# Performance work log

Hardware: AMD Instinct MI355X
Metric: run time of the kernel (lower is better)

Reference implementation:

```python
import jax, jax.numpy as jnp
import numpy as np

N_NODES = 100000
N_EDGES = 400000
F_IN = 128
HEADS = 4
C1 = 64   # conv1 out per head
C2 = 128  # conv2 out per head
G = 2048  # num graphs
FP = 2048
HID = 64
NEG_SLOPE = 0.2


def _gat_conv(x, edge_index, W, a_src, a_dst, b, heads, ch):
    """PyG-style GATConv with self-loops, concat=True."""
    n = x.shape[0]
    loops = jnp.arange(n, dtype=edge_index.dtype)
    src = jnp.concatenate([edge_index[0], loops])
    dst = jnp.concatenate([edge_index[1], loops])
    h = (x @ W).reshape(n, heads, ch)                      # [N,H,C]
    e_src = jnp.sum(h * a_src, axis=-1)                    # [N,H]
    e_dst = jnp.sum(h * a_dst, axis=-1)                    # [N,H]
    logits = jax.nn.leaky_relu(e_src[src] + e_dst[dst], NEG_SLOPE)  # [E,H]
    m = jax.ops.segment_max(logits, dst, num_segments=n)   # per-dst max
    p = jnp.exp(logits - m[dst])
    denom = jax.ops.segment_sum(p, dst, num_segments=n)
    alpha = p / denom[dst]                                 # [E,H]
    out = jax.ops.segment_sum(h[src] * alpha[:, :, None], dst, num_segments=n)
    return out.reshape(n, heads * ch) + b


def setup_inputs() -> dict:
    key = jax.random.key(0)
    ks = jax.random.split(key, 16)
    s = 0.05
    inp = {
        "x": jax.random.normal(ks[0], (N_NODES, F_IN), jnp.float32),
        "edge_index": jax.random.randint(ks[1], (2, N_EDGES), 0, N_NODES, jnp.int32),
        "batch": jnp.sort(jax.random.randint(ks[2], (N_NODES,), 0, G, jnp.int32)),
        "fp": jax.random.normal(ks[3], (G, FP), jnp.float32),
        "W1": jax.random.normal(ks[4], (F_IN, HEADS * C1), jnp.float32) * s,
        "a_src1": jax.random.normal(ks[5], (HEADS, C1), jnp.float32) * s,
        "a_dst1": jax.random.normal(ks[6], (HEADS, C1), jnp.float32) * s,
        "b1": jnp.zeros((HEADS * C1,), jnp.float32),
        "W2": jax.random.normal(ks[7], (HEADS * C1, HEADS * C2), jnp.float32) * s,
        "a_src2": jax.random.normal(ks[8], (HEADS, C2), jnp.float32) * s,
        "a_dst2": jax.random.normal(ks[9], (HEADS, C2), jnp.float32) * s,
        "b2": jnp.zeros((HEADS * C2,), jnp.float32),
        "Wfp": jax.random.normal(ks[10], (FP, HID), jnp.float32) * s,
        "bfp": jnp.zeros((HID,), jnp.float32),
        "Wfc1": jax.random.normal(ks[11], (HEADS * C2 + HID, HID), jnp.float32) * s,
        "bfc1": jnp.zeros((HID,), jnp.float32),
        "Wfc2": jax.random.normal(ks[12], (HID, 1), jnp.float32) * s,
        "bfc2": jnp.zeros((1,), jnp.float32),
    }
    return inp


def reference(x, edge_index, batch, fp, W1, a_src1, a_dst1, b1, W2, a_src2, a_dst2, b2,
              Wfp, bfp, Wfc1, bfc1, Wfc2, bfc2):
    h = _gat_conv(x, edge_index, W1, a_src1, a_dst1, b1, HEADS, C1)
    h = jax.nn.elu(h)
    h = _gat_conv(h, edge_index, W2, a_src2, a_dst2, b2, HEADS, C2)
    h = jax.nn.elu(h)
    # global mean pool over graphs
    sums = jax.ops.segment_sum(h, batch, num_segments=G)
    counts = jax.ops.segment_sum(jnp.ones((h.shape[0], 1), h.dtype), batch, num_segments=G)
    pooled = sums / jnp.maximum(counts, 1.0)               # [G, 512]
    fph = fp @ Wfp + bfp                                   # [G, 64]
    z = jnp.concatenate([pooled, fph], axis=1)             # [G, 576]
    z = jax.nn.relu(z @ Wfc1 + bfc1)
    # dropout is identity in eval mode
    return z @ Wfc2 + bfc2                                 # [G, 1]
```

## Files before the change

### kernel.cpp

```cpp
#include <hip/hip_runtime.h>
#include <math.h>

#define NEG_SLOPE 0.2f

typedef __attribute__((ext_vector_type(8))) short bf16x8;
typedef __attribute__((ext_vector_type(4))) float f32x4;
typedef __attribute__((ext_vector_type(2))) float f32x2;

__device__ __forceinline__ float b2f(short s) {
  return __uint_as_float(((unsigned int)(unsigned short)s) << 16);
}
__device__ __forceinline__ unsigned short f2b_rne(float f) {
  unsigned int u = __float_as_uint(f);
  u = (u + 0x7FFF + ((u >> 16) & 1)) >> 16;
  return (unsigned short)u;
}

__device__ __forceinline__ void fp8x8_to_f32(uint2 raw, float* f) {
  f32x2 a = __builtin_amdgcn_cvt_pk_f32_fp8((int)raw.x, false);
  f32x2 b = __builtin_amdgcn_cvt_pk_f32_fp8((int)raw.x, true);
  f32x2 c = __builtin_amdgcn_cvt_pk_f32_fp8((int)raw.y, false);
  f32x2 d = __builtin_amdgcn_cvt_pk_f32_fp8((int)raw.y, true);
  f[0] = a[0]; f[1] = a[1]; f[2] = b[0]; f[3] = b[1];
  f[4] = c[0]; f[5] = c[1]; f[6] = d[0]; f[7] = d[1];
}

__device__ __forceinline__ void tr_one(const float* __restrict__ W,
                                       unsigned short* __restrict__ WT,
                                       int K, int N, int idx)
{
  if (idx < K * N) {
    int k = idx / N, n = idx - k * N;
    WT[(size_t)n * K + k] = f2b_rne(W[idx]);
  }
}

__global__ __launch_bounds__(256) void prep_all(
    const float* __restrict__ x, unsigned short* __restrict__ xb, size_t nx, int B0,
    const float* __restrict__ fp, unsigned short* __restrict__ fpb, size_t nf, int B1,
    const float* __restrict__ W1, unsigned short* __restrict__ W1T,
    const float* __restrict__ W2, unsigned short* __restrict__ W2T,
    const float* __restrict__ Wfp, unsigned short* __restrict__ WfpT,
    const float* __restrict__ Wfc1, unsigned short* __restrict__ Wfc1T)
{
  int b = blockIdx.x;
  const int t = threadIdx.x;
  if (b < B0) {
    size_t i = (size_t)b * 256 + t;
    if (i < nx) xb[i] = f2b_rne(x[i]);
    return;
  }
  b -= B0;
  if (b < B1) {
    size_t i = (size_t)b * 256 + t;
    if (i < nf) fpb[i] = f2b_rne(fp[i]);
    return;
  }
  b -= B1;
  if (b < 128) { tr_one(W1, W1T, 128, 256, b * 256 + t); return; }
  b -= 128;
  if (b < 512) { tr_one(W2, W2T, 256, 512, b * 256 + t); return; }
  b -= 512;
  if (b < 512) { tr_one(Wfp, WfpT, 2048, 64, b * 256 + t); return; }
  b -= 512;
  tr_one(Wfc1, Wfc1T, 576, 64, b * 256 + t);
}

template<int EMODE>
__global__ __launch_bounds__(256) void gemm_mfma(
    const unsigned short* __restrict__ A, const unsigned short* __restrict__ BT,
    unsigned char* __restrict__ Cout, int M, int N, int K,
    const float* __restrict__ a_src, const float* __restrict__ a_dst,
    float* __restrict__ es, float* __restrict__ ed, int nh)
{
  const int LDT = 40;
  __shared__ unsigned short As[128 * 40];
  __shared__ unsigned short Bs[128 * 40];
  const int tid  = threadIdx.x;
  const int wave = tid >> 6;
  const int lane = tid & 63;
  const int ln   = lane & 15;
  const int quad = lane >> 4;
  const int wr0  = (wave >> 1) * 64;
  const int wc0  = (wave & 1) * 64;
  const int bm   = blockIdx.y * 128;
  const int bn   = blockIdx.x * 128;
  const int srow  = tid >> 2;
  const int skoff = (tid & 3) * 8;

  f32x4 acc[4][4];
  const f32x4 z4 = {0.f, 0.f, 0.f, 0.f};
#pragma unroll
  for (int i = 0; i < 4; ++i)
#pragma unroll
    for (int j = 0; j < 4; ++j) acc[i][j] = z4;

  const bf16x8 zb8 = {0, 0, 0, 0, 0, 0, 0, 0};
  bf16x8 pa[2] = {zb8, zb8}, pb[2] = {zb8, zb8};
  bf16x8 na[2] = {zb8, zb8}, nb[2] = {zb8, zb8};
#pragma unroll
  for (int p = 0; p < 2; ++p) {
    int r = srow + p * 64;
    pa[p] = (bm + r < M) ? *(const bf16x8*)(A + (size_t)(bm + r) * K + skoff) : zb8;
    pb[p] = *(const bf16x8*)(BT + (size_t)(bn + r) * K + skoff);
  }

  for (int k0 = 0; k0 < K; k0 += 32) {
#pragma unroll
    for (int p = 0; p < 2; ++p) {
      int r = srow + p * 64;
      *(bf16x8*)(&As[r * LDT + skoff]) = pa[p];
      *(bf16x8*)(&Bs[r * LDT + skoff]) = pb[p];
    }
    __syncthreads();
    if (k0 + 32 < K) {
      int kn = k0 + 32;
#pragma unroll
      for (int p = 0; p < 2; ++p) {
        int r = srow + p * 64;
        na[p] = (bm + r < M) ? *(const bf16x8*)(A + (size_t)(bm + r) * K + kn + skoff) : zb8;
        nb[p] = *(const bf16x8*)(BT + (size_t)(bn + r) * K + kn + skoff);
      }
    }
    bf16x8 af[4], bfv[4];
#pragma unroll
    for (int i = 0; i < 4; ++i)
      af[i] = *(const bf16x8*)(&As[(wr0 + i * 16 + ln) * LDT + quad * 8]);
#pragma unroll
    for (int j = 0; j < 4; ++j)
      bfv[j] = *(const bf16x8*)(&Bs[(wc0 + j * 16 + ln) * LDT + quad * 8]);
#pragma unroll
    for (int i = 0; i < 4; ++i)
#pragma unroll
      for (int j = 0; j < 4; ++j)
        acc[i][j] = __builtin_amdgcn_mfma_f32_16x16x32_bf16(af[i], bfv[j], acc[i][j], 0, 0, 0);
    __syncthreads();
#pragma unroll
    for (int p = 0; p < 2; ++p) { pa[p] = na[p]; pb[p] = nb[p]; }
  }

#pragma unroll
  for (int i = 0; i < 4; ++i) {
#pragma unroll
    for (int r = 0; r < 4; ++r) {
      int row = bm + wr0 + i * 16 + quad * 4 + r;
      if (row >= M) continue;
      int p01 = __builtin_amdgcn_cvt_pk_fp8_f32(acc[i][0][r], acc[i][1][r], 0, false);
      int p23 = __builtin_amdgcn_cvt_pk_fp8_f32(acc[i][2][r], acc[i][3][r], 0, false);
      size_t rb = (size_t)row * N + bn + wc0 + ln;
      Cout[rb +  0] = (unsigned char)(p01 & 0xff);
      Cout[rb + 16] = (unsigned char)((p01 >> 8) & 0xff);
      Cout[rb + 32] = (unsigned char)(p23 & 0xff);
      Cout[rb + 48] = (unsigned char)((p23 >> 8) & 0xff);
    }
  }

  float asv[4], adv[4];
#pragma unroll
  for (int j = 0; j < 4; ++j) {
    int col = bn + wc0 + j * 16 + ln;
    asv[j] = a_src[col];
    adv[j] = a_dst[col];
  }
  if (EMODE == 64) {
    const int head = (bn + wc0) >> 6;
#pragma unroll
    for (int i = 0; i < 4; ++i) {
#pragma unroll
      for (int r = 0; r < 4; ++r) {
        float ps = 0.f, pd = 0.f;
#pragma unroll
        for (int j = 0; j < 4; ++j) {
          ps = fmaf(acc[i][j][r], asv[j], ps);
          pd = fmaf(acc[i][j][r], adv[j], pd);
        }
        for (int off = 8; off; off >>= 1) {
          ps += __shfl_down(ps, off, 16);
          pd += __shfl_down(pd, off, 16);
        }
        if (ln == 0) {
          int row = bm + wr0 + i * 16 + quad * 4 + r;
          if (row < M) {
            es[(size_t)row * nh + head] = ps;
            ed[(size_t)row * nh + head] = pd;
          }
        }
      }
    }
  } else {
    float* esp = (float*)As;
    float* edp = esp + 256;
#pragma unroll
    for (int i = 0; i < 4; ++i) {
#pragma unroll
      for (int r = 0; r < 4; ++r) {
        float ps = 0.f, pd = 0.f;
#pragma unroll
        for (int j = 0; j < 4; ++j) {
          ps = fmaf(acc[i][j][r], asv[j], ps);
          pd = fmaf(acc[i][j][r], adv[j], pd);
        }
        for (int off = 8; off; off >>= 1) {
          ps += __shfl_down(ps, off, 16);
          pd += __shfl_down(pd, off, 16);
        }
        if (ln == 0) {
          int rl = wr0 + i * 16 + quad * 4 + r;
          esp[rl * 2 + (wc0 >> 6)] = ps;
          edp[rl * 2 + (wc0 >> 6)] = pd;
        }
      }
    }
    __syncthreads();
    if (tid < 128) {
      int row = bm + tid;
      if (row < M) {
        int head = bn >> 7;
        es[(size_t)row * nh + head] = esp[tid * 2] + esp[tid * 2 + 1];
        ed[(size_t)row * nh + head] = edp[tid * 2] + edp[tid * 2 + 1];
      }
    }
  }
}

__global__ __launch_bounds__(256) void gemm_mfma_n64(
    const unsigned short* __restrict__ A, int lda,
    const unsigned short* __restrict__ BT, int ldb,
    float* __restrict__ Cp, int M, int kchunk)
{
  const int LDT = 72;
  __shared__ unsigned short As[128 * 72];
  __shared__ unsigned short Bs[64 * 72];
  const int tid  = threadIdx.x;
  const int wave = tid >> 6;
  const int lane = tid & 63;
  const int ln   = lane & 15;
  const int quad = lane >> 4;
  const int ks   = blockIdx.x;
  const int bm   = blockIdx.y * 128;
  const int k_beg = ks * kchunk;
  const int k_end = k_beg + kchunk;
  const int arow = tid >> 1;
  const int akb  = (tid & 1) * 32;
  const int brow = tid >> 2;
  const int bkb  = (tid & 3) * 16;

  f32x4 acc[2][4];
  const f32x4 z4 = {0.f, 0.f, 0.f, 0.f};
#pragma unroll
  for (int i = 0; i < 2; ++i)
#pragma unroll
    for (int j = 0; j < 4; ++j) acc[i][j] = z4;

  for (int k0 = k_beg; k0 < k_end; k0 += 64) {
    const unsigned short* ap = A + (size_t)(bm + arow) * lda + k0 + akb;
#pragma unroll
    for (int q = 0; q < 4; ++q)
      *(bf16x8*)(&As[arow * LDT + akb + q * 8]) = *(const bf16x8*)(ap + q * 8);
    const unsigned short* bp = BT + (size_t)brow * ldb + k0 + bkb;
#pragma unroll
    for (int q = 0; q < 2; ++q)
      *(bf16x8*)(&Bs[brow * LDT + bkb + q * 8]) = *(const bf16x8*)(bp + q * 8);
    __syncthreads();
#pragma unroll
    for (int kk = 0; kk < 2; ++kk) {
      bf16x8 af[2], bfv[4];
#pragma unroll
      for (int i = 0; i < 2; ++i)
        af[i] = *(const bf16x8*)(&As[(wave * 32 + i * 16 + ln) * LDT + kk * 32 + quad * 8]);
#pragma unroll
      for (int j = 0; j < 4; ++j)
        bfv[j] = *(const bf16x8*)(&Bs[(j * 16 + ln) * LDT + kk * 32 + quad * 8]);
#pragma unroll
      for (int i = 0; i < 2; ++i)
#pragma unroll
        for (int j = 0; j < 4; ++j)
          acc[i][j] = __builtin_amdgcn_mfma_f32_16x16x32_bf16(af[i], bfv[j], acc[i][j], 0, 0, 0);
    }
    __syncthreads();
  }
#pragma unroll
  for (int i = 0; i < 2; ++i)
#pragma unroll
    for (int r = 0; r < 4; ++r) {
      int row = bm + wave * 32 + i * 16 + quad * 4 + r;
#pragma unroll
      for (int j = 0; j < 4; ++j)
        Cp[((size_t)ks * M + row) * 64 + j * 16 + ln] = acc[i][j][r];
    }
}

__global__ void fp_finish(const float* __restrict__ Cp, int ksplit, int M,
                          const float* __restrict__ bfp,
                          unsigned short* __restrict__ zb)
{
  const int g = blockIdx.x;
  const int j = threadIdx.x;
  float s = bfp[j];
  for (int ks = 0; ks < ksplit; ++ks) s += Cp[((size_t)ks * M + g) * 64 + j];
  zb[(size_t)g * 576 + 512 + j] = f2b_rne(s);
}

__global__ void mlp_finish(const float* __restrict__ Cp, int ksplit, int M,
                           const float* __restrict__ bfc1,
                           const float* __restrict__ Wfc2, const float* __restrict__ bfc2,
                           float* __restrict__ out)
{
  const int g = blockIdx.x;
  const int j = threadIdx.x;
  float s = bfc1[j];
  for (int ks = 0; ks < ksplit; ++ks) s += Cp[((size_t)ks * M + g) * 64 + j];
  s = s > 0.f ? s : 0.f;
  float term = s * Wfc2[j];
  for (int off = 32; off; off >>= 1) term += __shfl_down(term, off, 64);
  if (j == 0) out[g] = term + bfc2[0];
}

__global__ void count_all(const int* __restrict__ ei, int E, int* __restrict__ deg,
                          const int* __restrict__ batch, int NN, int* __restrict__ gcnt,
                          int BE)
{
  int b = blockIdx.x;
  int t = threadIdx.x;
  if (b < BE) {
    int e = b * 256 + t;
    if (e < E) atomicAdd(&deg[ei[E + e]], 1);
  } else {
    int i = (b - BE) * 256 + t;
    if (i < NN) atomicAdd(&gcnt[batch[i]], 1);
  }
}

__global__ void fill_csr(const int* __restrict__ ei, int E, int* __restrict__ cursor,
                         const int* __restrict__ rowptr, int* __restrict__ csr_src)
{
  int e = blockIdx.x * 256 + threadIdx.x;
  if (e < E) {
    int d = ei[E + e];
    int pos = atomicAdd(&cursor[d], 1);
    csr_src[rowptr[d] + pos] = ei[e];
  }
}

__device__ void scan_p1_body(const int* __restrict__ vals, int n, int* __restrict__ bsum,
                             int bb)
{
  __shared__ int red[256];
  int base = bb * 1024;
  int t = threadIdx.x;
  int s = 0;
#pragma unroll
  for (int i = 0; i < 4; ++i) {
    int idx = base + i * 256 + t;
    if (idx < n) s += vals[idx];
  }
  red[t] = s;
  __syncthreads();
  for (int off = 128; off; off >>= 1) {
    if (t < off) red[t] += red[t + off];
    __syncthreads();
  }
  if (t == 0) bsum[bb] = red[0];
}

__global__ void scan2_p1(const int* __restrict__ vA, int nA, int* __restrict__ bsA, int nbA,
                         const int* __restrict__ vB, int nB, int* __restrict__ bsB)
{
  int b = blockIdx.x;
  if (b < nbA) scan_p1_body(vA, nA, bsA, b);
  else         scan_p1_body(vB, nB, bsB, b - nbA);
}

__device__ void scan_p2_body(const int* __restrict__ bsum, int* __restrict__ bpre,
                             int nb, int* __restrict__ rowptr, int n)
{
  __shared__ int tmp[128];
  int t = threadIdx.x;
  int v = (t < nb) ? bsum[t] : 0;
  tmp[t] = v;
  __syncthreads();
  for (int off = 1; off < 128; off <<= 1) {
    int add = (t >= off) ? tmp[t - off] : 0;
    __syncthreads();
    tmp[t] += add;
    __syncthreads();
  }
  if (t < nb) bpre[t] = tmp[t] - v;
  if (t == 127) rowptr[n] = tmp[127];
}

__global__ void scan2_p2(const int* __restrict__ bsA, int* __restrict__ bpA, int nbA,
                         int* __restrict__ rpA, int nA,
                         const int* __restrict__ bsB, int* __restrict__ bpB, int nbB,
                         int* __restrict__ rpB, int nB)
{
  if (blockIdx.x == 0) scan_p2_body(bsA, bpA, nbA, rpA, nA);
  else                 scan_p2_body(bsB, bpB, nbB, rpB, nB);
}

__device__ void scan_p3_body(const int* __restrict__ vals, const int* __restrict__ bpre,
                             int n, int* __restrict__ rowptr, int bb)
{
  __shared__ int tmp[256];
  int t = threadIdx.x;
  int base = bb * 1024 + t * 4;
  int v[4]; int s = 0;
#pragma unroll
  for (int i = 0; i < 4; ++i) {
    int idx = base + i;
    v[i] = (idx < n) ? vals[idx] : 0;
    s += v[i];
  }
  tmp[t] = s;
  __syncthreads();
  for (int off = 1; off < 256; off <<= 1) {
    int add = (t >= off) ? tmp[t - off] : 0;
    __syncthreads();
    tmp[t] += add;
    __syncthreads();
  }
  int run = bpre[bb] + tmp[t] - s;
#pragma unroll
  for (int i = 0; i < 4; ++i) {
    int idx = base + i;
    if (idx < n) rowptr[idx] = run;
    run += v[i];
  }
}

__global__ void scan2_p3(const int* __restrict__ vA, const int* __restrict__ bpA, int nA,
                         int* __restrict__ rpA, int nbA,
                         const int* __restrict__ vB, const int* __restrict__ bpB, int nB,
                         int* __restrict__ rpB)
{
  int b = blockIdx.x;
  if (b < nbA) scan_p3_body(vA, bpA, nA, rpA, b);
  else         scan_p3_body(vB, bpB, nB, rpB, b - nbA);
}

__global__ void alpha_kernel(const float* __restrict__ es, const float* __restrict__ ed,
                             const int* __restrict__ rowptr, const int* __restrict__ csr_src,
                             float* __restrict__ w_csr, float* __restrict__ wself,
                             float* __restrict__ dinv, int N, int nh)
{
  int idx = blockIdx.x * 256 + threadIdx.x;
  if (idx >= N * nh) return;
  const int dst = idx / nh;
  const int h = idx - dst * nh;
  const float edh = ed[(size_t)dst * nh + h];
  const int beg = rowptr[dst], end = rowptr[dst + 1];
  float sum = 0.f;
  for (int e = beg; e < end; ++e) {
    int s = csr_src[e];
    float l = es[(size_t)s * nh + h] + edh;
    l = l >= 0.f ? l : NEG_SLOPE * l;
    float w = expf(l);
    w_csr[(size_t)e * nh + h] = w;
    sum += w;
  }
  float ls = es[(size_t)dst * nh + h] + edh;
  ls = ls >= 0.f ? ls : NEG_SLOPE * ls;
  float wsl = expf(ls);
  sum += wsl;
  wself[(size_t)dst * nh + h] = wsl;
  dinv[(size_t)dst * nh + h] = 1.0f / sum;
}

__global__ __launch_bounds__(256) void aggregate_b(
    const unsigned char* __restrict__ h,
    const float* __restrict__ w_csr, const float* __restrict__ wself,
    const float* __restrict__ dinv,
    const int* __restrict__ rowptr, const int* __restrict__ csr_src,
    const float* __restrict__ bias, unsigned short* __restrict__ out,
    int N, int nh, int C)
{
  const int HC = nh * C;
  const int CH8 = HC >> 3;
  const int dpb = 256 / CH8;
  const int grp = threadIdx.x / CH8;
  const int lane = threadIdx.x - grp * CH8;
  const int dst = blockIdx.x * dpb + grp;
  if (dst >= N) return;
  const int ch = lane << 3;
  const int head = ch / C;
  const int beg = rowptr[dst], end = rowptr[dst + 1];
  float acc[8] = {0.f, 0.f, 0.f, 0.f, 0.f, 0.f, 0.f, 0.f};
  float hv[8];
  int e = beg;
  for (; e + 1 < end; e += 2) {
    int s0 = csr_src[e], s1 = csr_src[e + 1];
    float a0 = w_csr[(size_t)e * nh + head];
    float a1 = w_csr[(size_t)(e + 1) * nh + head];
    uint2 r0 = *(const uint2*)(h + (size_t)s0 * HC + ch);
    uint2 r1 = *(const uint2*)(h + (size_t)s1 * HC + ch);
    fp8x8_to_f32(r0, hv);
#pragma unroll
    for (int r = 0; r < 8; ++r) acc[r] = fmaf(a0, hv[r], acc[r]);
    fp8x8_to_f32(r1, hv);
#pragma unroll
    for (int r = 0; r < 8; ++r) acc[r] = fmaf(a1, hv[r], acc[r]);
  }
  if (e < end) {
    int s0 = csr_src[e];
    float a0 = w_csr[(size_t)e * nh + head];
    uint2 r0 = *(const uint2*)(h + (size_t)s0 * HC + ch);
    fp8x8_to_f32(r0, hv);
#pragma unroll
    for (int r = 0; r < 8; ++r) acc[r] = fmaf(a0, hv[r], acc[r]);
  }
  {
    float a = wself[(size_t)dst * nh + head];
    uint2 r0 = *(const uint2*)(h + (size_t)dst * HC + ch);
    fp8x8_to_f32(r0, hv);
#pragma unroll
    for (int r = 0; r < 8; ++r) acc[r] = fmaf(a, hv[r], acc[r]);
  }
  const float di = dinv[(size_t)dst * nh + head];
  bf16x8 o;
#pragma unroll
  for (int r = 0; r < 8; ++r) {
    float v = acc[r] * di + bias[ch + r];
    v = v > 0.f ? v : (expf(v) - 1.0f);
    o[r] = (short)f2b_rne(v);
  }
  *(bf16x8*)(out + (size_t)dst * HC + ch) = o;
}

__global__ __launch_bounds__(256) void agg_pool(
    const unsigned char* __restrict__ h,
    const float* __restrict__ w_csr, const float* __restrict__ wself,
    const float* __restrict__ dinv,
    const int* __restrict__ rowptr, const int* __restrict__ csr_src,
    const float* __restrict__ bias, const int* __restrict__ grp,
    unsigned short* __restrict__ zb)
{
  const int g = blockIdx.x;
  const int wave = threadIdx.x >> 6;
  const int lane = threadIdx.x & 63;
  const int ch = lane << 3;
  const int head = lane >> 4;
  const int gbeg = grp[g], gend = grp[g + 1];
  float bch[8];
#pragma unroll
  for (int r = 0; r < 8; ++r) bch[r] = bias[ch + r];
  float pool[8] = {0.f, 0.f, 0.f, 0.f, 0.f, 0.f, 0.f, 0.f};
  float hv[8];

  for (int node = gbeg + wave; node < gend; node += 4) {
    const int beg = rowptr[node], end = rowptr[node + 1];
    float acc[8] = {0.f, 0.f, 0.f, 0.f, 0.f, 0.f, 0.f, 0.f};
    int e = beg;
    for (; e + 1 < end; e += 2) {
      int s0 = csr_src[e], s1 = csr_src[e + 1];
      float a0 = w_csr[(size_t)e * 4 + head];
      float a1 = w_csr[(size_t)(e + 1) * 4 + head];
      uint2 r0 = *(const uint2*)(h + (size_t)s0 * 512 + ch);
      uint2 r1 = *(const uint2*)(h + (size_t)s1 * 512 + ch);
      fp8x8_to_f32(r0, hv);
#pragma unroll
      for (int r = 0; r < 8; ++r) acc[r] = fmaf(a0, hv[r], acc[r]);
      fp8x8_to_f32(r1, hv);
#pragma unroll
      for (int r = 0; r < 8; ++r) acc[r] = fmaf(a1, hv[r], acc[r]);
    }
    if (e < end) {
      int s0 = csr_src[e];
      float a0 = w_csr[(size_t)e * 4 + head];
      uint2 r0 = *(const uint2*)(h + (size_t)s0 * 512 + ch);
      fp8x8_to_f32(r0, hv);
#pragma unroll
      for (int r = 0; r < 8; ++r) acc[r] = fmaf(a0, hv[r], acc[r]);
    }
    {
      float a = wself[(size_t)node * 4 + head];
      uint2 r0 = *(const uint2*)(h + (size_t)node * 512 + ch);
      fp8x8_to_f32(r0, hv);
#pragma unroll
      for (int r = 0; r < 8; ++r) acc[r] = fmaf(a, hv[r], acc[r]);
    }
    const float di = dinv[(size_t)node * 4 + head];
#pragma unroll
    for (int r = 0; r < 8; ++r) {
      float v = acc[r] * di + bch[r];
      v = v > 0.f ? v : (expf(v) - 1.0f);
      pool[r] += v;
    }
  }

  __shared__ float red[4][512];
#pragma unroll
  for (int r = 0; r < 8; ++r) red[wave][ch + r] = pool[r];
  __syncthreads();
  const float inv = 1.0f / (float)max(gend - gbeg, 1);
#pragma unroll
  for (int k = 0; k < 2; ++k) {
    int c = threadIdx.x + k * 256;
    float s = (red[0][c] + red[1][c]) + (red[2][c] + red[3][c]);
    zb[(size_t)g * 576 + c] = f2b_rne(s * inv);
  }
}

extern "C" void kernel_launch(void* const* d_in, const int* in_sizes, int n_in,
                              void* d_out, int out_size, void* d_ws, size_t ws_size,
                              hipStream_t stream)
{
  const float* x      = (const float*)d_in[0];
  const int*   ei     = (const int*)d_in[1];
  const int*   batch  = (const int*)d_in[2];
  const float* fp     = (const float*)d_in[3];
  const float* W1     = (const float*)d_in[4];
  const float* a_src1 = (const float*)d_in[5];
  const float* a_dst1 = (const float*)d_in[6];
  const float* b1     = (const float*)d_in[7];
  const float* W2     = (const float*)d_in[8];
  const float* a_src2 = (const float*)d_in[9];
  const float* a_dst2 = (const float*)d_in[10];
  const float* b2     = (const float*)d_in[11];
  const float* Wfp    = (const float*)d_in[12];
  const float* bfp    = (const float*)d_in[13];
  const float* Wfc1   = (const float*)d_in[14];
  const float* bfc1   = (const float*)d_in[15];
  const float* Wfc2   = (const float*)d_in[16];
  const float* bfc2   = (const float*)d_in[17];
  float* out = (float*)d_out;

  const int NN = in_sizes[0] / 128;
  const int E  = in_sizes[1] / 2;
  const int G  = in_sizes[3] / 2048;
  const int FIN = 128, H = 4, C1 = 64, C2 = 128;
  const int HC1 = H * C1;
  const int HC2 = H * C2;
  const int KFP = in_sizes[3] / G;
  const int KZ  = HC2 + 64;
  const int KS_FP = 16;
  const int KS_Z  = 9;

  char* base = (char*)d_ws;
  size_t off = 0;
  auto alloc = [&](size_t bytes) {
    char* p = base + off; off += (bytes + 255) & ~(size_t)255; return p;
  };
  size_t xb_sz  = ((size_t)NN * FIN * 2 + 255) & ~(size_t)255;
  size_t h1b_sz = (size_t)NN * HC1;
  size_t h2b_sz = (size_t)NN * HC2;
  size_t rA = xb_sz + h1b_sz; if (h2b_sz > rA) rA = h2b_sz;
  char* RA = alloc(rA);
  unsigned short* xb  = (unsigned short*)RA;
  unsigned char*  h1b = (unsigned char*)(RA + xb_sz);
  unsigned char*  h2b = (unsigned char*)RA;
  size_t fpb_sz  = ((size_t)G * KFP * 2 + 255) & ~(size_t)255;
  size_t cpfp_sz = (size_t)KS_FP * G * 64 * 4;
  size_t agg1_sz = (size_t)NN * HC1 * 2;
  size_t rB = fpb_sz + cpfp_sz; if (agg1_sz > rB) rB = agg1_sz;
  char* RB = alloc(rB);
  unsigned short* fpb   = (unsigned short*)RB;
  float*          Cp_fp = (float*)(RB + fpb_sz);
  unsigned short* agg1b = (unsigned short*)RB;
  float* w1     = (float*)alloc((size_t)E * H * 4);
  float* wself1 = (float*)alloc((size_t)NN * H * 4);
  float* es1    = (float*)alloc((size_t)NN * H * 4);
  float* ed1    = (float*)alloc((size_t)NN * H * 4);
  float* dinv1  = (float*)alloc((size_t)NN * H * 4);
  float* w2 = w1, *wself2 = wself1, *es2 = es1, *ed2 = ed1, *dinv2 = dinv1;
  unsigned short* zb    = (unsigned short*)alloc((size_t)G * KZ * 2);
  float*          Cp_z  = (float*)alloc((size_t)KS_Z * G * 64 * 4);
  unsigned short* W1T   = (unsigned short*)alloc((size_t)HC1 * FIN * 2);
  unsigned short* W2T   = (unsigned short*)alloc((size_t)HC2 * HC1 * 2);
  unsigned short* WfpT  = (unsigned short*)alloc((size_t)64 * KFP * 2);
  unsigned short* Wfc1T = (unsigned short*)alloc((size_t)64 * KZ * 2);
  int* iarena   = (int*)alloc(((size_t)2 * NN + G) * 4);
  int* deg      = iarena;
  int* cursor   = iarena + NN;
  int* gcnt     = iarena + 2 * NN;
  int* rowptr_n = (int*)alloc(((size_t)NN + 1) * 4);
  int* rowptr_g = (int*)alloc(((size_t)G + 1) * 4);
  int* csr_src  = (int*)alloc((size_t)E * 4);
  int* bsumA    = (int*)alloc(128 * 4);
  int* bpreA    = (int*)alloc(128 * 4);
  int* bsumB    = (int*)alloc(128 * 4);
  int* bpreB    = (int*)alloc(128 * 4);

  const size_t nx = (size_t)NN * FIN;
  const size_t nf = (size_t)G * KFP;
  const int B0 = (int)((nx + 255) / 256);
  const int B1 = (int)((nf + 255) / 256);
  {
    int nb = B0 + B1 + 128 + 512 + 512 + 144;
    prep_all<<<nb, 256, 0, stream>>>(x, xb, nx, B0, fp, fpb, nf, B1,
                                     W1, W1T, W2, W2T, Wfp, WfpT, Wfc1, Wfc1T);
  }

  {
    dim3 gg(KS_FP, G / 128);
    gemm_mfma_n64<<<gg, 256, 0, stream>>>(fpb, KFP, WfpT, KFP, Cp_fp, G, KFP / KS_FP);
    fp_finish<<<G, 64, 0, stream>>>(Cp_fp, KS_FP, G, bfp, zb);
  }

  hipMemsetAsync(iarena, 0, sizeof(int) * ((size_t)2 * NN + G), stream);
  {
    int BE = (E + 255) / 256;
    int BN = (NN + 255) / 256;
    count_all<<<BE + BN, 256, 0, stream>>>(ei, E, deg, batch, NN, gcnt, BE);
  }
  {
    int nbA = (NN + 1023) / 1024;
    int nbB = (G + 1023) / 1024;
    scan2_p1<<<nbA + nbB, 256, 0, stream>>>(deg, NN, bsumA, nbA, gcnt, G, bsumB);
    scan2_p2<<<2, 128, 0, stream>>>(bsumA, bpreA, nbA, rowptr_n, NN,
                                    bsumB, bpreB, nbB, rowptr_g, G);
    scan2_p3<<<nbA + nbB, 256, 0, stream>>>(deg, bpreA, NN, rowptr_n, nbA,
                                            gcnt, bpreB, G, rowptr_g);
  }
  fill_csr<<<(E + 255) / 256, 256, 0, stream>>>(ei, E, cursor, rowptr_n, csr_src);

  {
    dim3 gg(HC1 / 128, (NN + 127) / 128);
    gemm_mfma<64><<<gg, 256, 0, stream>>>(xb, W1T, h1b, NN, HC1, FIN,
                                          a_src1, a_dst1, es1, ed1, H);
  }
  alpha_kernel<<<(NN * H + 255) / 256, 256, 0, stream>>>(es1, ed1, rowptr_n, csr_src,
                                                         w1, wself1, dinv1, NN, H);
  aggregate_b<<<(NN + 7) / 8, 256, 0, stream>>>(h1b, w1, wself1, dinv1, rowptr_n, csr_src,
                                                b1, agg1b, NN, H, C1);

  {
    dim3 gg(HC2 / 128, (NN + 127) / 128);
    gemm_mfma<128><<<gg, 256, 0, stream>>>(agg1b, W2T, h2b, NN, HC2, HC1,
                                           a_src2, a_dst2, es2, ed2, H);
  }
  alpha_kernel<<<(NN * H + 255) / 256, 256, 0, stream>>>(es2, ed2, rowptr_n, csr_src,
                                                         w2, wself2, dinv2, NN, H);
  agg_pool<<<G, 256, 0, stream>>>(h2b, w2, wself2, dinv2, rowptr_n, csr_src,
                                  b2, rowptr_g, zb);

  {
    dim3 gg(KS_Z, G / 128);
    gemm_mfma_n64<<<gg, 256, 0, stream>>>(zb, KZ, Wfc1T, KZ, Cp_z, G, KZ / KS_Z);
    mlp_finish<<<G, 64, 0, stream>>>(Cp_z, KS_Z, G, bfc1, Wfc2, bfc2, out);
  }
}
```

Measured before the change: 456.5 us.

## Double-buffer GEMM tiles with direct global-to-LDS async loads

Replaces the register-staged global loads and LDS stores in the MFMA GEMM with global_load_lds direct-to-LDS copies into a double-buffered, unpadded shared tile. One __syncthreads per k-step replaces two, and the register prefetch copies are gone. Out-of-range A rows are clamped to the last row instead of zero-filled. The unpadded 32-element row stride may cause LDS bank conflicts on the fragment reads. Correctness relies on async LDS writes being visible after the barrier without an explicit vmcnt wait.

```diff
diff --git a/kernel.cpp b/kernel.cpp
--- a/kernel.cpp
+++ b/kernel.cpp
@@ -23,6 +23,12 @@
   f32x2 d = __builtin_amdgcn_cvt_pk_f32_fp8((int)raw.y, true);
   f[0] = a[0]; f[1] = a[1]; f[2] = b[0]; f[3] = b[1];
   f[4] = c[0]; f[5] = c[1]; f[6] = d[0]; f[7] = d[1];
+}
+
+__device__ __forceinline__ void gload16(const unsigned short* g, unsigned short* l) {
+  __builtin_amdgcn_global_load_lds(
+      (const __attribute__((address_space(1))) unsigned int*)g,
+      (__attribute__((address_space(3))) unsigned int*)l, 16, 0, 0);
 }
 
 __device__ __forceinline__ void tr_one(const float* __restrict__ W,
@@ -73,9 +79,8 @@
     const float* __restrict__ a_src, const float* __restrict__ a_dst,
     float* __restrict__ es, float* __restrict__ ed, int nh)
 {
-  const int LDT = 40;
-  __shared__ unsigned short As[128 * 40];
-  __shared__ unsigned short Bs[128 * 40];
+  __shared__ unsigned short As[2][128 * 32];
+  __shared__ unsigned short Bs[2][128 * 32];
   const int tid  = threadIdx.x;
   const int wave = tid >> 6;
   const int lane = tid & 63;
@@ -85,8 +90,17 @@
   const int wc0  = (wave & 1) * 64;
   const int bm   = blockIdx.y * 128;
   const int bn   = blockIdx.x * 128;
-  const int srow  = tid >> 2;
-  const int skoff = (tid & 3) * 8;
+
+  const int sr = lane >> 2;
+  const int sc = (lane & 3) * 8;
+  int arow0 = bm + wave * 32 + sr;
+  int arow1 = arow0 + 16;
+  if (arow0 >= M) arow0 = M - 1;
+  if (arow1 >= M) arow1 = M - 1;
+  const unsigned short* ga0 = A + (size_t)arow0 * K + sc;
+  const unsigned short* ga1 = A + (size_t)arow1 * K + sc;
+  const unsigned short* gb0 = BT + (size_t)(bn + wave * 32 + sr) * K + sc;
+  const unsigned short* gb1 = BT + (size_t)(bn + wave * 32 + 16 + sr) * K + sc;
 
   f32x4 acc[4][4];
   const f32x4 z4 = {0.f, 0.f, 0.f, 0.f};
@@ -95,49 +109,39 @@
 #pragma unroll
     for (int j = 0; j < 4; ++j) acc[i][j] = z4;
 
-  const bf16x8 zb8 = {0, 0, 0, 0, 0, 0, 0, 0};
-  bf16x8 pa[2] = {zb8, zb8}, pb[2] = {zb8, zb8};
-  bf16x8 na[2] = {zb8, zb8}, nb[2] = {zb8, zb8};
-#pragma unroll
-  for (int p = 0; p < 2; ++p) {
-    int r = srow + p * 64;
-    pa[p] = (bm + r < M) ? *(const bf16x8*)(A + (size_t)(bm + r) * K + skoff) : zb8;
-    pb[p] = *(const bf16x8*)(BT + (size_t)(bn + r) * K + skoff);
-  }
-
+  {
+    gload16(ga0, &As[0][wave * 1024]);
+    gload16(ga1, &As[0][wave * 1024 + 512]);
+    gload16(gb0, &Bs[0][wave * 1024]);
+    gload16(gb1, &Bs[0][wave * 1024 + 512]);
+  }
+
+  int cur = 0;
   for (int k0 = 0; k0 < K; k0 += 32) {
-#pragma unroll
-    for (int p = 0; p < 2; ++p) {
-      int r = srow + p * 64;
-      *(bf16x8*)(&As[r * LDT + skoff]) = pa[p];
-      *(bf16x8*)(&Bs[r * LDT + skoff]) = pb[p];
-    }
     __syncthreads();
     if (k0 + 32 < K) {
-      int kn = k0 + 32;
-#pragma unroll
-      for (int p = 0; p < 2; ++p) {
-        int r = srow + p * 64;
-        na[p] = (bm + r < M) ? *(const bf16x8*)(A + (size_t)(bm + r) * K + kn + skoff) : zb8;
-        nb[p] = *(const bf16x8*)(BT + (size_t)(bn + r) * K + kn + skoff);
-      }
+      const int kn = k0 + 32;
+      const int nb = cur ^ 1;
+      gload16(ga0 + kn, &As[nb][wave * 1024]);
+      gload16(ga1 + kn, &As[nb][wave * 1024 + 512]);
+      gload16(gb0 + kn, &Bs[nb][wave * 1024]);
+      gload16(gb1 + kn, &Bs[nb][wave * 1024 + 512]);
     }
     bf16x8 af[4], bfv[4];
 #pragma unroll
     for (int i = 0; i < 4; ++i)
-      af[i] = *(const bf16x8*)(&As[(wr0 + i * 16 + ln) * LDT + quad * 8]);
+      af[i] = *(const bf16x8*)(&As[cur][(wr0 + i * 16 + ln) * 32 + quad * 8]);
 #pragma unroll
     for (int j = 0; j < 4; ++j)
-      bfv[j] = *(const bf16x8*)(&Bs[(wc0 + j * 16 + ln) * LDT + quad * 8]);
+      bfv[j] = *(const bf16x8*)(&Bs[cur][(wc0 + j * 16 + ln) * 32 + quad * 8]);
 #pragma unroll
     for (int i = 0; i < 4; ++i)
 #pragma unroll
       for (int j = 0; j < 4; ++j)
         acc[i][j] = __builtin_amdgcn_mfma_f32_16x16x32_bf16(af[i], bfv[j], acc[i][j], 0, 0, 0);
-    __syncthreads();
-#pragma unroll
-    for (int p = 0; p < 2; ++p) { pa[p] = na[p]; pb[p] = nb[p]; }
-  }
+    cur ^= 1;
+  }
+  __syncthreads();
 
 #pragma unroll
   for (int i = 0; i < 4; ++i) {
@@ -188,7 +192,7 @@
       }
     }
   } else {
-    float* esp = (float*)As;
+    float* esp = (float*)As[0];
     float* edp = esp + 256;
 #pragma unroll
     for (int i = 0; i < 4; ++i) {
```

Result: no change. 459.6 us (+0.7%).
